# Optimization experiments

Hardware: AMD Instinct MI355X
Metric: run time of the kernel (lower is better)

## Reference

```python
import jax, jax.numpy as jnp
import numpy as np

V = 100277      # VOCAB_SIZE
SCR = 64        # SCRATCH_SLOTS
STEPS = 8       # MAX_STEPS_LIMIT
H = 8           # num_heads (hard-coded in UniversalReasoner)
NEG = -1e9


def _layernorm(x, s, b, eps=1e-6):
    mu = x.mean(-1, keepdims=True)
    var = ((x - mu) ** 2).mean(-1, keepdims=True)
    return (x - mu) * jax.lax.rsqrt(var + eps) * s + b


def setup_inputs() -> dict:
    key = jax.random.key(0)
    ks = jax.random.split(key, 16)
    D = 1024
    n = lambda k, shape, sc=0.02: jax.random.normal(k, shape, dtype=jnp.float32) * sc
    return {
        "tokens": jax.random.randint(ks[0], (16, 128), 0, V),
        "embed": n(ks[1], (V, D)),
        "time_embed": n(ks[2], (STEPS + 1, D)),
        "scratch": n(ks[3], (1, SCR, D)),
        "wq": n(ks[4], (D, D)), "bq": jnp.zeros((D,), jnp.float32),
        "wk": n(ks[5], (D, D)), "bk": jnp.zeros((D,), jnp.float32),
        "wv": n(ks[6], (D, D)), "bv": jnp.zeros((D,), jnp.float32),
        "wo": n(ks[7], (D, D)), "bo": jnp.zeros((D,), jnp.float32),
        "ln1_s": jnp.ones((D,), jnp.float32), "ln1_b": jnp.zeros((D,), jnp.float32),
        "ln2_s": jnp.ones((D,), jnp.float32), "ln2_b": jnp.zeros((D,), jnp.float32),
        "w1": n(ks[8], (D, 4 * D)), "b1": jnp.zeros((4 * D,), jnp.float32),
        "w2": n(ks[9], (4 * D, D)), "b2": jnp.zeros((D,), jnp.float32),
        "halt_w": n(ks[10], (D, 1)), "halt_b": jnp.zeros((1,), jnp.float32),
        "dec_w": n(ks[11], (D, V)), "dec_b": jnp.zeros((V,), jnp.float32),
    }


def reference(tokens, embed, time_embed, scratch, wq, bq, wk, bk, wv, bv, wo, bo,
              ln1_s, ln1_b, ln2_s, ln2_b, w1, b1, w2, b2, halt_w, halt_b, dec_w, dec_b):
    B, S = tokens.shape
    D = embed.shape[1]
    hd = D // H
    T = S + SCR                     # seq + scratch slots
    scale = hd ** -0.5

    # RoPE caches (matches 10000**(arange(0,hd,2)/hd) in the module)
    inv_freq = 1.0 / 10000.0 ** (jnp.arange(0, hd, 2, dtype=jnp.float32) / hd)
    t = jnp.arange(T, dtype=jnp.float32)
    freqs = jnp.outer(t, inv_freq)              # [T, hd/2]
    sin = jnp.sin(freqs); cos = jnp.cos(freqs)
    sin_ext = jnp.stack([sin, sin], -1).reshape(T, hd)[None, :, None, :]
    cos_ext = jnp.stack([cos, cos], -1).reshape(T, hd)[None, :, None, :]

    # hybrid mask: causal for the seq part, fully-visible rows for scratch tokens
    causal = jnp.tril(jnp.ones((T, T), dtype=bool))
    mask = causal.at[S:, :].set(True)[None, None, :, :]   # [1,1,T,T]

    def rotate(x):  # x: [B,T,H,hd]
        xe, xo = x[..., 0::2], x[..., 1::2]
        xr = jnp.stack([-xo, xe], -1).reshape(x.shape)
        return x * cos_ext + xr * sin_ext

    def block(x):   # one StandardReasoningBlock on [B,T,D]
        h = _layernorm(x, ln1_s, ln1_b)
        q = (h @ wq + bq).reshape(B, T, H, hd)
        k = (h @ wk + bk).reshape(B, T, H, hd)
        v = (h @ wv + bv).reshape(B, T, H, hd)
        q, k = rotate(q), rotate(k)
        logits = jnp.einsum('bshd,bthd->bhst', q, k) * scale
        logits = jnp.where(mask, logits, NEG)
        w = jax.nn.softmax(logits, axis=-1)
        o = jnp.einsum('bhst,bthd->bshd', w, v).reshape(B, T, D)
        x = x + (o @ wo + bo)
        h2 = _layernorm(x, ln2_s, ln2_b)
        x = x + jax.nn.gelu(h2 @ w1 + b1, approximate=True) @ w2 + b2
        return x

    z0 = jnp.concatenate([embed[tokens], jnp.tile(scratch, (B, 1, 1))], axis=1)  # [B,T,D]

    def step(z, i):
        zt = z + time_embed[i][None, None, :]
        nz = block(zt)
        halt = jax.nn.sigmoid((nz[:, S:, :] @ halt_w + halt_b).mean(axis=(1, 2)))  # [B]
        return nz, halt

    final_z, halts = jax.lax.scan(step, z0, jnp.arange(STEPS))   # halts: [STEPS, B]
    logits_out = final_z[:, :S, :] @ dec_w + dec_b               # [B,S,V]
    return logits_out, halts
```

## Files before the change

### kernel.cpp

```cpp
#include <hip/hip_runtime.h>
#include <hip/hip_bf16.h>
#include <math.h>


typedef float  f32x4  __attribute__((ext_vector_type(4)));
typedef __bf16 bf16x8 __attribute__((ext_vector_type(8)));
typedef __bf16 bf16x4 __attribute__((ext_vector_type(4)));

static constexpr int BB   = 16;
static constexpr int S    = 128;
static constexpr int SCR  = 64;
static constexpr int T    = 192;
static constexpr int D    = 1024;
static constexpr int H    = 8;
static constexpr int HD   = 128;
static constexpr int DFF  = 4096;
static constexpr int NSTEP= 8;
static constexpr int V    = 100277;
static constexpr int ROWS = BB * T;
static constexpr int MD   = BB * S;
static constexpr long long LOGITS = (long long)BB * S * V;
static constexpr size_t QSZ = (size_t)BB * H * T * HD;

#define DEV __device__ __forceinline__

DEV void gload16(const __bf16* g, __bf16* l) {
  __builtin_amdgcn_global_load_lds(
      (__attribute__((address_space(1))) void*)(g),
      (__attribute__((address_space(3))) void*)(l), 16, 0, 0);
}

template <int EPI>
__global__ __launch_bounds__(256) void k_gemm(
    const __bf16* __restrict__ A, long long sA, int ldA, int M,
    const __bf16* __restrict__ Bt, long long sB, int ldB, int N, int K,
    const float* __restrict__ bias, void* __restrict__ C, long long sC,
    int ldC, const float* __restrict__ rct, const float* __restrict__ rst) {
  const int bz = blockIdx.z;
  const __bf16* Ab;
  const __bf16* Bb;
  if constexpr (EPI == 4) {
    Ab = A + (size_t)bz * K;
    Bb = Bt + (size_t)bz * K;
  } else {
    Ab = A + (size_t)bz * sA;
    Bb = Bt + (size_t)bz * sB;
  }
  const int tm = blockIdx.y * 128, tn = blockIdx.x * 128;
  const int tid = threadIdx.x;
  const int lane = tid & 63, wv = tid >> 6;
  const int wr = wv >> 1, wc = wv & 1;

  __shared__ __bf16 As[2][128 * 32];
  __shared__ __bf16 Bs[2][128 * 32];

  f32x4 acc[4][4];
#pragma unroll
  for (int m = 0; m < 4; m++)
#pragma unroll
    for (int n = 0; n < 4; n++) acc[m][n] = (f32x4)(0.f);

  const int lrow = lane >> 2;
  const int lcol = (((lane & 3) ^ ((lrow >> 1) & 3)) * 8);
  int arow[2], brow[2];
#pragma unroll
  for (int c2 = 0; c2 < 2; c2++) {
    const int ch = wv * 2 + c2;
    int ar = tm + ch * 16 + lrow; if (ar > M - 1) ar = M - 1;
    int br = tn + ch * 16 + lrow; if (br > N - 1) br = N - 1;
    arow[c2] = ar; brow[c2] = br;
  }

  auto stage = [&](int buf, int kk) {
#pragma unroll
    for (int c2 = 0; c2 < 2; c2++) {
      const int ch = wv * 2 + c2;
      gload16(Ab + (size_t)arow[c2] * ldA + kk + lcol, &As[buf][ch * 512]);
      gload16(Bb + (size_t)brow[c2] * ldB + kk + lcol, &Bs[buf][ch * 512]);
    }
  };

  const int rsl = (((lane >> 4) ^ (((lane & 15) >> 1) & 3)) * 8);
  auto compute = [&](int cur) {
    bf16x8 af[4], bfv[4];
#pragma unroll
    for (int m = 0; m < 4; m++)
      af[m] = *(const bf16x8*)&As[cur][(wr * 64 + m * 16 + (lane & 15)) * 32 + rsl];
#pragma unroll
    for (int n = 0; n < 4; n++)
      bfv[n] = *(const bf16x8*)&Bs[cur][(wc * 64 + n * 16 + (lane & 15)) * 32 + rsl];
    asm volatile("s_waitcnt lgkmcnt(0)" ::: "memory");
    __builtin_amdgcn_sched_barrier(0);
    __builtin_amdgcn_s_barrier();
#pragma unroll
    for (int m = 0; m < 4; m++)
#pragma unroll
      for (int n = 0; n < 4; n++)
        acc[m][n] = __builtin_amdgcn_mfma_f32_16x16x32_bf16(af[m], bfv[n],
                                                            acc[m][n], 0, 0, 0);
  };

  const int niter = K >> 5;
  stage(0, 0);
  for (int it = 0; it < niter - 1; ++it) {
    const int cur = it & 1;
    stage(cur ^ 1, (it + 1) << 5);
    asm volatile("s_waitcnt vmcnt(4)" ::: "memory");
    __builtin_amdgcn_s_barrier();
    compute(cur);
  }
  asm volatile("s_waitcnt vmcnt(0)" ::: "memory");
  __builtin_amdgcn_s_barrier();
  compute((niter - 1) & 1);

  const int r0 = tm + wr * 64, c0 = tn + wc * 64;
  if constexpr (EPI == 5) {
    const int kind = tn >> 10;
#pragma unroll
    for (int n = 0; n < 4; n++) {
      const int c = c0 + n * 16 + (lane & 15);
      const int hh = (c & 1023) >> 7, d = c & 127, jp = d >> 1;
      const float bsv = bias[c];
#pragma unroll
      for (int m = 0; m < 4; m++) {
        const int rb = r0 + m * 16 + ((lane >> 4) << 2);
#pragma unroll
        for (int j = 0; j < 4; j++) {
          const int r = rb + j;
          const float x = acc[m][n][j] + bsv;
          const float xo = __shfl_xor(x, 1);
          const int b = r / T, t = r % T;
          if (kind == 2) {
            ((__bf16*)C)[2 * QSZ + ((size_t)((b * H + hh) * HD + d)) * T + t] =
                (__bf16)x;
          } else {
            const float cs = rct[t * 64 + jp], sn = rst[t * 64 + jp];
            const float o = (c & 1) ? (x * cs + xo * sn) : (x * cs - xo * sn);
            ((__bf16*)C)[(size_t)kind * QSZ +
                         ((size_t)((b * H + hh) * T + t)) * HD + d] = (__bf16)o;
          }
        }
      }
    }
    return;
  }
#pragma unroll
  for (int n = 0; n < 4; n++) {
    const int c = c0 + n * 16 + (lane & 15);
    if (c >= N) continue;
    const float bsv = (bias && (EPI != 4 || bz == 0)) ? bias[c] : 0.f;
#pragma unroll
    for (int m = 0; m < 4; m++) {
      const int rb = r0 + m * 16 + ((lane >> 4) << 2);
#pragma unroll
      for (int j = 0; j < 4; j++) {
        const int r = rb + j;
        if (r >= M) continue;
        float x = acc[m][n][j] + bsv;
        if constexpr (EPI == 4) {
          atomicAdd((float*)C + (size_t)r * ldC + c, x);
        } else {
          const size_t idx = (size_t)bz * sC + (size_t)r * ldC + c;
          if constexpr (EPI == 2) {
            const float u = x;
            const float gl =
                0.5f * u * (1.f + tanhf(0.7978845608f * (u + 0.044715f * u * u * u)));
            ((__bf16*)C)[idx] = (__bf16)gl;
          } else {
            ((float*)C)[idx] += x;
          }
        }
      }
    }
  }
}

__global__ __launch_bounds__(256) void k_attn(const __bf16* __restrict__ qb,
                                              const __bf16* __restrict__ kb,
                                              const __bf16* __restrict__ vT,
                                              __bf16* __restrict__ ob) {
  extern __shared__ char smem[];
  __bf16* Kl = (__bf16*)smem;
  __bf16* Pl = (__bf16*)smem;
  __bf16* Vl = (__bf16*)(smem + 73728);
  const int bh = blockIdx.x;
  const int tid = threadIdx.x, lane = tid & 63, wv = tid >> 6;
  const int g4 = lane >> 4, l15 = lane & 15;
  const size_t hoff = (size_t)bh * T * HD;
  const size_t voff = (size_t)bh * HD * T;

  bf16x8 qf[3][4];
#pragma unroll
  for (int m = 0; m < 3; m++)
#pragma unroll
    for (int ks = 0; ks < 4; ks++) {
      const int tq = wv * 48 + m * 16 + l15;
      qf[m][ks] = *(const bf16x8*)(qb + hoff + (size_t)tq * HD + ks * 32 + g4 * 8);
    }

#pragma unroll
  for (int ci = 0; ci < 12; ci++) {
    const int ch = wv * 12 + ci;
    const int grow = ch * 4 + g4;
    const int sl = l15 ^ (grow & 7);
    gload16(kb + hoff + (size_t)grow * HD + sl * 8, Kl + ch * 512);
  }
#pragma unroll
  for (int ci = 0; ci < 12; ci++) {
    const int ch = wv * 12 + ci;
    const int c = ch >> 4, ch2 = ch & 15;
    const int d = ch2 * 8 + (lane >> 3);
    const int sl = (lane & 7) ^ (d & 7);
    gload16(vT + voff + (size_t)d * T + c * 64 + sl * 8,
            Vl + c * 8192 + ch2 * 512);
  }
  asm volatile("s_waitcnt vmcnt(0)" ::: "memory");
  __builtin_amdgcn_s_barrier();

  f32x4 sacc[3][12];
#pragma unroll
  for (int m = 0; m < 3; m++)
#pragma unroll
    for (int nf = 0; nf < 12; nf++) sacc[m][nf] = (f32x4)(0.f);
#pragma unroll
  for (int ks = 0; ks < 4; ks++)
#pragma unroll
    for (int nf = 0; nf < 12; nf++) {
      const int row = nf * 16 + l15;
      const int sl = (ks * 4 + g4) ^ (row & 7);
      const bf16x8 kf = *(const bf16x8*)&Kl[row * 128 + sl * 8];
#pragma unroll
      for (int m = 0; m < 3; m++)
        sacc[m][nf] = __builtin_amdgcn_mfma_f32_16x16x32_bf16(qf[m][ks], kf,
                                                              sacc[m][nf], 0, 0, 0);
    }

  const float scale = 0.08838834764831845f;
  float inv[3][4];
#pragma unroll
  for (int m = 0; m < 3; m++)
#pragma unroll
    for (int j = 0; j < 4; j++) {
      const int tq = wv * 48 + m * 16 + g4 * 4 + j;
#pragma unroll
      for (int nf = 0; nf < 12; nf++) {
        const int c = nf * 16 + l15;
        float v = sacc[m][nf][j] * scale;
        if (tq < S && c > tq) v = -1e30f;
        sacc[m][nf][j] = v;
      }
      float mm = -1e30f;
#pragma unroll
      for (int nf = 0; nf < 12; nf++) mm = fmaxf(mm, sacc[m][nf][j]);
#pragma unroll
      for (int o = 1; o < 16; o <<= 1) mm = fmaxf(mm, __shfl_xor(mm, o));
      float sum = 0.f;
#pragma unroll
      for (int nf = 0; nf < 12; nf++) {
        const float e = __expf(sacc[m][nf][j] - mm);
        sacc[m][nf][j] = e;
        sum += e;
      }
#pragma unroll
      for (int o = 1; o < 16; o <<= 1) sum += __shfl_xor(sum, o);
      inv[m][j] = 1.f / sum;
    }

  __builtin_amdgcn_s_barrier();
#pragma unroll
  for (int m = 0; m < 3; m++)
#pragma unroll
    for (int nf = 0; nf < 12; nf++)
#pragma unroll
      for (int j = 0; j < 4; j++) {
        const int q = wv * 48 + m * 16 + g4 * 4 + j;
        const int c = nf * 16 + l15;
        Pl[q * 192 + (((c >> 3) ^ (q & 7)) * 8) + (c & 7)] =
            (__bf16)(sacc[m][nf][j] * inv[m][j]);
      }
  asm volatile("s_waitcnt lgkmcnt(0)" ::: "memory");
  __builtin_amdgcn_sched_barrier(0);

  f32x4 oacc[3][8];
#pragma unroll
  for (int m = 0; m < 3; m++)
#pragma unroll
    for (int nf = 0; nf < 8; nf++) oacc[m][nf] = (f32x4)(0.f);
#pragma unroll
  for (int ks = 0; ks < 6; ks++) {
    bf16x8 pf[3];
#pragma unroll
    for (int m = 0; m < 3; m++) {
      const int q = wv * 48 + m * 16 + l15;
      const int sl = (ks * 4 + g4) ^ (q & 7);
      pf[m] = *(const bf16x8*)&Pl[q * 192 + sl * 8];
    }
#pragma unroll
    for (int nf = 0; nf < 8; nf++) {
      const int d = nf * 16 + l15;
      const int sl = ((ks & 1) * 4 + g4) ^ (d & 7);
      const bf16x8 vf = *(const bf16x8*)&Vl[(ks >> 1) * 8192 + d * 64 + sl * 8];
#pragma unroll
      for (int m = 0; m < 3; m++)
        oacc[m][nf] = __builtin_amdgcn_mfma_f32_16x16x32_bf16(pf[m], vf,
                                                              oacc[m][nf], 0, 0, 0);
    }
  }

  const int b = bh >> 3, hh = bh & 7;
#pragma unroll
  for (int m = 0; m < 3; m++)
#pragma unroll
    for (int nf = 0; nf < 8; nf++) {
      const int d = nf * 16 + l15;
#pragma unroll
      for (int j = 0; j < 4; j++) {
        const int tq = wv * 48 + m * 16 + g4 * 4 + j;
        ob[((size_t)(b * T + tq)) * D + hh * HD + d] = (__bf16)oacc[m][nf][j];
      }
    }
}

static constexpr int DEC_NT = (V + 127) / 128;
static constexpr int DEC_NWG = 16 * DEC_NT;

__global__ __launch_bounds__(256) void k_dec(const __bf16* __restrict__ A,
                                             const __bf16* __restrict__ Bt,
                                             const float* __restrict__ bias,
                                             float* __restrict__ C) {
  const int bid = blockIdx.x;
  const int swz = (bid & 7) * (DEC_NWG / 8) + (bid >> 3);
  const int tm = (swz & 15) * 128, tn = (swz >> 4) * 128;
  const int tid = threadIdx.x;
  const int lane = tid & 63, wv = tid >> 6;
  const int wr = wv >> 1, wc = wv & 1;

  __shared__ __bf16 sAB[2][2][4096];
  float* cbuf = (float*)sAB;

  f32x4 acc[4][4];
#pragma unroll
  for (int m = 0; m < 4; m++)
#pragma unroll
    for (int n = 0; n < 4; n++) acc[m][n] = (f32x4)(0.f);

  const int lrow = lane >> 2;
  const int lcol = (((lane & 3) ^ ((lrow >> 1) & 3)) * 8);
  int arow[2], brow[2];
#pragma unroll
  for (int c2 = 0; c2 < 2; c2++) {
    const int ch = wv * 2 + c2;
    arow[c2] = tm + ch * 16 + lrow;
    int br = tn + ch * 16 + lrow; if (br > V - 1) br = V - 1;
    brow[c2] = br;
  }

  auto stage = [&](int buf, int kk) {
#pragma unroll
    for (int c2 = 0; c2 < 2; c2++) {
      const int ch = wv * 2 + c2;
      gload16(A + (size_t)arow[c2] * D + kk + lcol, &sAB[buf][0][ch * 512]);
      gload16(Bt + (size_t)brow[c2] * D + kk + lcol, &sAB[buf][1][ch * 512]);
    }
  };

  const int rsl = (((lane >> 4) ^ (((lane & 15) >> 1) & 3)) * 8);
  auto compute = [&](int cur) {
    bf16x8 af[4], bfv[4];
#pragma unroll
    for (int m = 0; m < 4; m++)
      af[m] = *(const bf16x8*)&sAB[cur][0][(wr * 64 + m * 16 + (lane & 15)) * 32 + rsl];
#pragma unroll
    for (int n = 0; n < 4; n++)
      bfv[n] = *(const bf16x8*)&sAB[cur][1][(wc * 64 + n * 16 + (lane & 15)) * 32 + rsl];
    asm volatile("s_waitcnt lgkmcnt(0)" ::: "memory");
    __builtin_amdgcn_sched_barrier(0);
    __builtin_amdgcn_s_barrier();
#pragma unroll
    for (int m = 0; m < 4; m++)
#pragma unroll
      for (int n = 0; n < 4; n++)
        acc[m][n] = __builtin_amdgcn_mfma_f32_16x16x32_bf16(af[m], bfv[n],
                                                            acc[m][n], 0, 0, 0);
  };

  stage(0, 0);
  for (int it = 0; it < D / 32 - 1; ++it) {
    const int cur = it & 1;
    stage(cur ^ 1, (it + 1) << 5);
    asm volatile("s_waitcnt vmcnt(4)" ::: "memory");
    __builtin_amdgcn_s_barrier();
    compute(cur);
  }
  asm volatile("s_waitcnt vmcnt(0)" ::: "memory");
  __builtin_amdgcn_s_barrier();
  compute((D / 32 - 1) & 1);
  __syncthreads();

  const int l15 = lane & 15, g4 = lane >> 4;
  const bool full = (tn + 128 <= V);
  for (int pass = 0; pass < 2; ++pass) {
    if (pass) __syncthreads();
    if (wr == pass) {
#pragma unroll
      for (int n = 0; n < 4; n++) {
        const int col = wc * 64 + n * 16 + l15;
        const float bsv = (tn + col < V) ? bias[tn + col] : 0.f;
#pragma unroll
        for (int m = 0; m < 4; m++) {
#pragma unroll
          for (int j = 0; j < 4; j++) {
            const int row = m * 16 + g4 * 4 + j;
            const int slot = (col >> 2) ^ (row & 7);
            cbuf[row * 128 + slot * 4 + (col & 3)] = acc[m][n][j] + bsv;
          }
        }
      }
    }
    __syncthreads();
    const int rbase = tm + pass * 64;
    if (full) {
      const int c8 = tid & 7;
#pragma unroll
      for (int rr = 0; rr < 2; ++rr) {
        const int row = rr * 32 + (tid >> 3);
#pragma unroll
        for (int i = 0; i < 4; ++i) {
          const int ps = (c8 ^ (row & 7)) + i * 8;
          const f32x4 v = *(const f32x4*)&cbuf[row * 128 + ps * 4];
          __builtin_nontemporal_store(
              v, (f32x4*)&C[(size_t)(rbase + row) * V + tn + (c8 + i * 8) * 4]);
        }
      }
    } else {
      for (int idx = tid; idx < 64 * 128; idx += 256) {
        const int row = idx >> 7, col = idx & 127;
        if (tn + col < V)
          __builtin_nontemporal_store(
              cbuf[row * 128 + (((col >> 2) ^ (row & 7)) << 2) + (col & 3)],
              &C[(size_t)(rbase + row) * V + tn + col]);
      }
    }
  }
}

__global__ __launch_bounds__(256) void k_transpose(const float* __restrict__ in,
                                                   __bf16* __restrict__ out,
                                                   int R, int C) {
  __shared__ __bf16 tile[32][33];
  const int c0 = blockIdx.x * 32, r0 = blockIdx.y * 32;
  const int tx = threadIdx.x & 31, ty = threadIdx.x >> 5;
#pragma unroll
  for (int i = 0; i < 32; i += 8) {
    const int r = r0 + ty + i, c = c0 + tx;
    tile[ty + i][tx] = (r < R && c < C) ? (__bf16)in[(size_t)r * C + c] : (__bf16)0.f;
  }
  __syncthreads();
  const int oc = threadIdx.x >> 3, rch = (threadIdx.x & 7) * 4;
  const int occ = c0 + oc, orr = r0 + rch;
  if (occ < C && orr + 3 < R) {
    bf16x4 v;
#pragma unroll
    for (int j = 0; j < 4; j++) v[j] = tile[rch + j][oc];
    *(bf16x4*)(out + (size_t)occ * R + orr) = v;
  }
}

__global__ __launch_bounds__(256) void k_concat_bias(const float* bq,
                                                     const float* bk,
                                                     const float* bv,
                                                     float* out) {
  const int i = blockIdx.x * 256 + threadIdx.x;
  if (i < D) { out[i] = bq[i]; out[D + i] = bk[i]; out[2 * D + i] = bv[i]; }
}

__global__ __launch_bounds__(256) void k_rope_table(float* __restrict__ ct,
                                                    float* __restrict__ st) {
  const int i = blockIdx.x * 256 + threadIdx.x;
  if (i < T * 64) {
    const int t = i >> 6, j = i & 63;
    const float inv = expf(-((float)(2 * j) * (1.f / 128.f)) * 9.210340371976184f);
    const float ang = (float)t * inv;
    ct[i] = cosf(ang);
    st[i] = sinf(ang);
  }
}

__global__ __launch_bounds__(256) void k_build_z(const int* __restrict__ tokens,
                                                 const float* __restrict__ embed,
                                                 const float* __restrict__ scratch,
                                                 float* __restrict__ z) {
  const int row = blockIdx.x;
  const int b = row / T, t = row % T;
  const float* src = (t < S) ? embed + (size_t)tokens[b * S + t] * D
                             : scratch + (size_t)(t - S) * D;
  ((float4*)(z + (size_t)row * D))[threadIdx.x] =
      ((const float4*)src)[threadIdx.x];
}

template <bool ADDT>
__global__ __launch_bounds__(256) void k_ln(float* __restrict__ z,
                                            const float* __restrict__ te,
                                            const float* __restrict__ gs,
                                            const float* __restrict__ gb,
                                            __bf16* __restrict__ h) {
  const int row = blockIdx.x, tid = threadIdx.x;
  float* zp = z + (size_t)row * D;
  float4 x = ((float4*)zp)[tid];
  if (ADDT) {
    const float4 t4 = ((const float4*)te)[tid];
    x.x += t4.x; x.y += t4.y; x.z += t4.z; x.w += t4.w;
    ((float4*)zp)[tid] = x;
  }
  float s = x.x + x.y + x.z + x.w;
  float s2 = x.x * x.x + x.y * x.y + x.z * x.z + x.w * x.w;
#pragma unroll
  for (int o = 32; o; o >>= 1) { s += __shfl_xor(s, o); s2 += __shfl_xor(s2, o); }
  __shared__ float rs[4], rq[4];
  const int wv = tid >> 6, ln = tid & 63;
  if (!ln) { rs[wv] = s; rq[wv] = s2; }
  __syncthreads();
  s = rs[0] + rs[1] + rs[2] + rs[3];
  s2 = rq[0] + rq[1] + rq[2] + rq[3];
  const float mu = s * (1.f / D);
  const float var = s2 * (1.f / D) - mu * mu;
  const float rinv = 1.0f / sqrtf(var + 1e-6f);
  const int c = tid * 4;
  const float4 g4 = ((const float4*)gs)[tid];
  const float4 b4 = ((const float4*)gb)[tid];
  bf16x4 o4;
  o4[0] = (__bf16)((x.x - mu) * rinv * g4.x + b4.x);
  o4[1] = (__bf16)((x.y - mu) * rinv * g4.y + b4.y);
  o4[2] = (__bf16)((x.z - mu) * rinv * g4.z + b4.z);
  o4[3] = (__bf16)((x.w - mu) * rinv * g4.w + b4.w);
  *(bf16x4*)(h + (size_t)row * D + c) = o4;
}

__global__ __launch_bounds__(256) void k_halt(const float* __restrict__ z,
                                              const float* __restrict__ hw,
                                              const float* __restrict__ hb,
                                              float* __restrict__ out) {
  const int b = blockIdx.x, tid = threadIdx.x;
  const float4 w4 = ((const float4*)hw)[tid];
  float acc = 0.f;
  for (int j = 0; j < SCR; j++) {
    const float4 x = ((const float4*)(z + ((size_t)(b * T + S + j)) * D))[tid];
    acc += x.x * w4.x + x.y * w4.y + x.z * w4.z + x.w * w4.w;
  }
#pragma unroll
  for (int o = 32; o; o >>= 1) acc += __shfl_xor(acc, o);
  __shared__ float rs[4];
  const int wv = tid >> 6, ln = tid & 63;
  if (!ln) rs[wv] = acc;
  __syncthreads();
  if (tid == 0) {
    const float tot = rs[0] + rs[1] + rs[2] + rs[3];
    out[b] = 1.f / (1.f + expf(-(tot * (1.f / SCR) + hb[0])));
  }
}

__global__ __launch_bounds__(256) void k_cast(const float* __restrict__ z,
                                              __bf16* __restrict__ zb) {
  const int row = blockIdx.x;
  const int b = row >> 7, s = row & 127;
  const float4 x = ((const float4*)(z + ((size_t)(b * T + s)) * D))[threadIdx.x];
  bf16x4 o;
  o[0] = (__bf16)x.x; o[1] = (__bf16)x.y; o[2] = (__bf16)x.z; o[3] = (__bf16)x.w;
  *(bf16x4*)(zb + (size_t)row * D + threadIdx.x * 4) = o;
}

extern "C" void kernel_launch(void* const* d_in, const int* in_sizes, int n_in,
                              void* d_out, int out_size, void* d_ws,
                              size_t ws_size, hipStream_t stream) {
  const int* tokens = (const int*)d_in[0];
  const float* embed = (const float*)d_in[1];
  const float* time_embed = (const float*)d_in[2];
  const float* scratch = (const float*)d_in[3];
  const float* wq = (const float*)d_in[4];  const float* bq = (const float*)d_in[5];
  const float* wk = (const float*)d_in[6];  const float* bk = (const float*)d_in[7];
  const float* wvv = (const float*)d_in[8]; const float* bv = (const float*)d_in[9];
  const float* wo = (const float*)d_in[10]; const float* bo = (const float*)d_in[11];
  const float* ln1s = (const float*)d_in[12]; const float* ln1b = (const float*)d_in[13];
  const float* ln2s = (const float*)d_in[14]; const float* ln2b = (const float*)d_in[15];
  const float* w1 = (const float*)d_in[16]; const float* b1 = (const float*)d_in[17];
  const float* w2 = (const float*)d_in[18]; const float* b2 = (const float*)d_in[19];
  const float* hw = (const float*)d_in[20]; const float* hb = (const float*)d_in[21];
  const float* dw = (const float*)d_in[22]; const float* db = (const float*)d_in[23];

  char* w = (char*)d_ws;
  size_t off = 0;
  auto al = [&](size_t n) { size_t o = off; off += (n + 255) & ~(size_t)255; return o; };
  const size_t oWqkvT = al((size_t)3 * D * D * 2);
  const size_t oWoT   = al((size_t)D * D * 2);
  const size_t oW1T   = al((size_t)DFF * D * 2);
  const size_t oW2T   = al((size_t)D * DFF * 2);
  const size_t oDecT  = al((size_t)V * D * 2);
  const size_t oBqkv  = al((size_t)3 * D * 4);
  const size_t oCt    = al((size_t)T * 64 * 4);
  const size_t oSt    = al((size_t)T * 64 * 4);
  const size_t oZ     = al((size_t)ROWS * D * 4);
  const size_t oH     = al((size_t)ROWS * D * 2);
  const size_t oG     = al((size_t)ROWS * DFF * 2);
  const size_t oOB    = al((size_t)ROWS * D * 2);
  const size_t oQ     = al(QSZ * 2);
  const size_t oK     = al(QSZ * 2);
  const size_t oVT    = al(QSZ * 2);
  (void)ws_size; (void)in_sizes; (void)n_in; (void)out_size;

  __bf16* WqkvT = (__bf16*)(w + oWqkvT);
  __bf16* WoT   = (__bf16*)(w + oWoT);
  __bf16* W1T   = (__bf16*)(w + oW1T);
  __bf16* W2T   = (__bf16*)(w + oW2T);
  __bf16* DecT  = (__bf16*)(w + oDecT);
  float*  bqkv  = (float*)(w + oBqkv);
  float*  ct    = (float*)(w + oCt);
  float*  st    = (float*)(w + oSt);
  float*  z     = (float*)(w + oZ);
  __bf16* h     = (__bf16*)(w + oH);
  __bf16* g     = (__bf16*)(w + oG);
  __bf16* ob    = (__bf16*)(w + oOB);
  __bf16* qb    = (__bf16*)(w + oQ);
  __bf16* kb    = (__bf16*)(w + oK);
  __bf16* vT    = (__bf16*)(w + oVT);
  __bf16* zb    = (__bf16*)(w + oH);

  float* logits = (float*)d_out;
  float* halts  = (float*)d_out + LOGITS;

  k_transpose<<<dim3(32, 32), 256, 0, stream>>>(wq, WqkvT, D, D);
  k_transpose<<<dim3(32, 32), 256, 0, stream>>>(wk, WqkvT + (size_t)D * D, D, D);
  k_transpose<<<dim3(32, 32), 256, 0, stream>>>(wvv, WqkvT + (size_t)2 * D * D, D, D);
  k_transpose<<<dim3(32, 32), 256, 0, stream>>>(wo, WoT, D, D);
  k_transpose<<<dim3(128, 32), 256, 0, stream>>>(w1, W1T, D, DFF);
  k_transpose<<<dim3(32, 128), 256, 0, stream>>>(w2, W2T, DFF, D);
  k_transpose<<<dim3((V + 31) / 32, 32), 256, 0, stream>>>(dw, DecT, D, V);
  k_concat_bias<<<4, 256, 0, stream>>>(bq, bk, bv, bqkv);
  k_rope_table<<<(T * 64 + 255) / 256, 256, 0, stream>>>(ct, st);
  k_build_z<<<ROWS, 256, 0, stream>>>(tokens, embed, scratch, z);

  for (int step = 0; step < NSTEP; step++) {
    k_ln<true><<<ROWS, 256, 0, stream>>>(z, time_embed + (size_t)step * D, ln1s, ln1b, h);
    k_gemm<5><<<dim3(24, 24, 1), 256, 0, stream>>>(h, 0, D, ROWS, WqkvT, 0, D,
                                                   3 * D, D, bqkv, qb, 0, 0, ct, st);
    k_attn<<<BB * H, 256, 122880, stream>>>(qb, kb, vT, ob);
    k_gemm<1><<<dim3(8, 24, 1), 256, 0, stream>>>(ob, 0, D, ROWS, WoT, 0, D, D,
                                                  D, bo, z, 0, D, nullptr, nullptr);
    k_ln<false><<<ROWS, 256, 0, stream>>>(z, nullptr, ln2s, ln2b, h);
    k_gemm<2><<<dim3(32, 24, 1), 256, 0, stream>>>(h, 0, D, ROWS, W1T, 0, D,
                                                   DFF, D, b1, g, 0, DFF, nullptr, nullptr);
    k_gemm<4><<<dim3(8, 24, 4), 256, 0, stream>>>(g, 0, DFF, ROWS, W2T, 0, DFF,
                                                  D, DFF / 4, b2, z, 0, D, nullptr, nullptr);
    k_halt<<<BB, 256, 0, stream>>>(z, hw, hb, halts + step * BB);
  }

  k_cast<<<MD, 256, 0, stream>>>(z, zb);
  k_dec<<<DEC_NWG, 256, 0, stream>>>(zb, DecT, db, logits);
}
```

Measured before the change: 2.956 ms.

## Enlarge decoder GEMM tile to 256x256 with 512-thread workgroups

The vocabulary-projection GEMM moves from 128x128 tiles with 4 waves to 256x256 tiles with 8 waves. Each wave now computes a 128x64 sub-tile, which raises operand reuse and halves the number of workgroups re-reading the activation and weight panels. The epilogue is rewritten to write four 64-row passes through shared memory, and plain stores replace the nontemporal stores. The 128-float accumulator per thread under launch_bounds(512,2) puts heavy pressure on registers and may spill. Dropping the nontemporal hint could also change cache behaviour for the very large logits write.

New measurement: 2.798 ms. 1.06x faster.

```diff
diff --git a/kernel.cpp b/kernel.cpp
--- a/kernel.cpp
+++ b/kernel.cpp
@@ -321,63 +321,62 @@
     }
 }
 
-static constexpr int DEC_NT = (V + 127) / 128;
-static constexpr int DEC_NWG = 16 * DEC_NT;
-
-__global__ __launch_bounds__(256) void k_dec(const __bf16* __restrict__ A,
-                                             const __bf16* __restrict__ Bt,
-                                             const float* __restrict__ bias,
-                                             float* __restrict__ C) {
+static constexpr int DEC_NT = (V + 255) / 256;
+static constexpr int DEC_NWG = 8 * DEC_NT;
+
+__global__ __launch_bounds__(512, 2) void k_dec(const __bf16* __restrict__ A,
+                                                const __bf16* __restrict__ Bt,
+                                                const float* __restrict__ bias,
+                                                float* __restrict__ C) {
   const int bid = blockIdx.x;
-  const int swz = (bid & 7) * (DEC_NWG / 8) + (bid >> 3);
-  const int tm = (swz & 15) * 128, tn = (swz >> 4) * 128;
+  const int swz = (bid & 7) * DEC_NT + (bid >> 3);
+  const int tm = (swz & 7) * 256, tn = (swz >> 3) * 256;
   const int tid = threadIdx.x;
   const int lane = tid & 63, wv = tid >> 6;
-  const int wr = wv >> 1, wc = wv & 1;
-
-  __shared__ __bf16 sAB[2][2][4096];
+  const int wm = wv >> 2, wn = wv & 3;
+  const int g4 = lane >> 4, l15 = lane & 15;
+
+  __shared__ __bf16 sAB[2][2][8192];
   float* cbuf = (float*)sAB;
 
-  f32x4 acc[4][4];
-#pragma unroll
-  for (int m = 0; m < 4; m++)
+  f32x4 acc[8][4];
+#pragma unroll
+  for (int m = 0; m < 8; m++)
 #pragma unroll
     for (int n = 0; n < 4; n++) acc[m][n] = (f32x4)(0.f);
 
-  const int lrow = lane >> 2;
-  const int lcol = (((lane & 3) ^ ((lrow >> 1) & 3)) * 8);
-  int arow[2], brow[2];
-#pragma unroll
-  for (int c2 = 0; c2 < 2; c2++) {
-    const int ch = wv * 2 + c2;
-    arow[c2] = tm + ch * 16 + lrow;
-    int br = tn + ch * 16 + lrow; if (br > V - 1) br = V - 1;
-    brow[c2] = br;
-  }
+  const int trow = tid >> 2, t4 = tid & 3;
+  const int pcol = ((t4 ^ ((trow >> 1) & 3)) * 8);
+  const int ar0 = tm + trow, ar1 = tm + 128 + trow;
+  int br0 = tn + trow;       if (br0 > V - 1) br0 = V - 1;
+  int br1 = tn + 128 + trow; if (br1 > V - 1) br1 = V - 1;
 
   auto stage = [&](int buf, int kk) {
-#pragma unroll
-    for (int c2 = 0; c2 < 2; c2++) {
-      const int ch = wv * 2 + c2;
-      gload16(A + (size_t)arow[c2] * D + kk + lcol, &sAB[buf][0][ch * 512]);
-      gload16(Bt + (size_t)brow[c2] * D + kk + lcol, &sAB[buf][1][ch * 512]);
-    }
+    gload16(A + (size_t)ar0 * D + kk + pcol, &sAB[buf][0][(size_t)tid * 8]);
+    gload16(A + (size_t)ar1 * D + kk + pcol, &sAB[buf][0][4096 + (size_t)tid * 8]);
+    gload16(Bt + (size_t)br0 * D + kk + pcol, &sAB[buf][1][(size_t)tid * 8]);
+    gload16(Bt + (size_t)br1 * D + kk + pcol, &sAB[buf][1][4096 + (size_t)tid * 8]);
   };
 
-  const int rsl = (((lane >> 4) ^ (((lane & 15) >> 1) & 3)) * 8);
   auto compute = [&](int cur) {
-    bf16x8 af[4], bfv[4];
-#pragma unroll
-    for (int m = 0; m < 4; m++)
-      af[m] = *(const bf16x8*)&sAB[cur][0][(wr * 64 + m * 16 + (lane & 15)) * 32 + rsl];
-#pragma unroll
-    for (int n = 0; n < 4; n++)
-      bfv[n] = *(const bf16x8*)&sAB[cur][1][(wc * 64 + n * 16 + (lane & 15)) * 32 + rsl];
+    bf16x8 af[8], bfv[4];
+#pragma unroll
+    for (int m = 0; m < 8; m++) {
+      const int row = wm * 128 + m * 16 + l15;
+      const int ps = g4 ^ ((row >> 1) & 3);
+      af[m] = *(const bf16x8*)&sAB[cur][0][row * 32 + ps * 8];
+    }
+#pragma unroll
+    for (int n = 0; n < 4; n++) {
+      const int row = wn * 64 + n * 16 + l15;
+      const int ps = g4 ^ ((row >> 1) & 3);
+      bfv[n] = *(const bf16x8*)&sAB[cur][1][row * 32 + ps * 8];
+    }
     asm volatile("s_waitcnt lgkmcnt(0)" ::: "memory");
     __builtin_amdgcn_sched_barrier(0);
     __builtin_amdgcn_s_barrier();
 #pragma unroll
-    for (int m = 0; m < 4; m++)
+    for (int m = 0; m < 8; m++)
 #pragma unroll
       for (int n = 0; n < 4; n++)
         acc[m][n] = __builtin_amdgcn_mfma_f32_16x16x32_bf16(af[m], bfv[n],
@@ -397,22 +396,22 @@
   compute((D / 32 - 1) & 1);
   __syncthreads();
 
-  const int l15 = lane & 15, g4 = lane >> 4;
-  const bool full = (tn + 128 <= V);
-  for (int pass = 0; pass < 2; ++pass) {
+  const bool full = (tn + 256 <= V);
+  for (int pass = 0; pass < 4; ++pass) {
     if (pass) __syncthreads();
-    if (wr == pass) {
+    if (wm == (pass >> 1)) {
+      const int mfb = (pass & 1) * 4;
 #pragma unroll
       for (int n = 0; n < 4; n++) {
-        const int col = wc * 64 + n * 16 + l15;
+        const int col = wn * 64 + n * 16 + l15;
         const float bsv = (tn + col < V) ? bias[tn + col] : 0.f;
 #pragma unroll
-        for (int m = 0; m < 4; m++) {
+        for (int m2 = 0; m2 < 4; m2++) {
 #pragma unroll
           for (int j = 0; j < 4; j++) {
-            const int row = m * 16 + g4 * 4 + j;
-            const int slot = (col >> 2) ^ (row & 7);
-            cbuf[row * 128 + slot * 4 + (col & 3)] = acc[m][n][j] + bsv;
+            const int row = m2 * 16 + g4 * 4 + j;
+            const int phys = (col >> 2) ^ (row & 7);
+            cbuf[row * 256 + phys * 4 + (col & 3)] = acc[mfb + m2][n][j] + bsv;
           }
         }
       }
@@ -420,25 +419,19 @@
     __syncthreads();
     const int rbase = tm + pass * 64;
     if (full) {
-      const int c8 = tid & 7;
-#pragma unroll
-      for (int rr = 0; rr < 2; ++rr) {
-        const int row = rr * 32 + (tid >> 3);
-#pragma unroll
-        for (int i = 0; i < 4; ++i) {
-          const int ps = (c8 ^ (row & 7)) + i * 8;
-          const f32x4 v = *(const f32x4*)&cbuf[row * 128 + ps * 4];
-          __builtin_nontemporal_store(
-              v, (f32x4*)&C[(size_t)(rbase + row) * V + tn + (c8 + i * 8) * 4]);
-        }
+      const int row = tid >> 3, c8 = tid & 7;
+#pragma unroll
+      for (int i = 0; i < 8; ++i) {
+        const int ps = (c8 ^ (row & 7)) + i * 8;
+        const f32x4 v = *(const f32x4*)&cbuf[row * 256 + ps * 4];
+        *(f32x4*)&C[(size_t)(rbase + row) * V + tn + (c8 + i * 8) * 4] = v;
       }
     } else {
-      for (int idx = tid; idx < 64 * 128; idx += 256) {
-        const int row = idx >> 7, col = idx & 127;
+      for (int idx = tid; idx < 64 * 256; idx += 512) {
+        const int row = idx >> 8, col = idx & 255;
         if (tn + col < V)
-          __builtin_nontemporal_store(
-              cbuf[row * 128 + (((col >> 2) ^ (row & 7)) << 2) + (col & 3)],
-              &C[(size_t)(rbase + row) * V + tn + col]);
+          C[(size_t)(rbase + row) * V + tn + col] =
+              cbuf[row * 256 + (((col >> 2) ^ (row & 7)) << 2) + (col & 3)];
       }
     }
   }
@@ -654,5 +647,5 @@
   }
 
   k_cast<<<MD, 256, 0, stream>>>(z, zb);
-  k_dec<<<DEC_NWG, 256, 0, stream>>>(zb, DecT, db, logits);
-}
+  k_dec<<<DEC_NWG, 512, 0, stream>>>(zb, DecT, db, logits);
+}
```
